# Optimization experiments

Hardware: AMD Instinct MI355X
Metric: run time of the kernel (lower is better)

## Reference

```python
import jax, jax.numpy as jnp
import numpy as np
import math

B, N, M = 128, 16, 32
D_OBS, D_OUT = 128, 128            # obs_input_dim, obs_output_dim (== obs_output_dim_other)
D_OA, D_AV = 136, 128              # obs_act_input_dim, obs_act_output_dim
D_OBS_O, D_OA_O, D_AV_O = 128, 136, 128
D_FINAL_IN, D_HID, D_FINAL_OUT = 256, 64, 1
N_ACT = 8


def setup_inputs() -> dict:
    key = jax.random.key(0)
    ks = jax.random.split(key, 16)
    s = 0.05
    return {
        "states": jax.random.normal(ks[0], (B, N, D_OBS), jnp.float32),
        "policies": jax.random.uniform(ks[1], (B, N, N_ACT), jnp.float32),
        "actions": jax.random.uniform(ks[2], (B, N, N_ACT), jnp.float32),
        "states_other": jax.random.normal(ks[3], (B, M, D_OBS_O), jnp.float32),
        "actions_other": jax.random.uniform(ks[4], (B, M, N_ACT), jnp.float32),
        # weights stored as [in, out] (torch Linear applies x @ W.T)
        "Wk": jax.random.normal(ks[5], (D_OBS, D_OUT), jnp.float32) * s,
        "Wq": jax.random.normal(ks[6], (D_OBS, D_OUT), jnp.float32) * s,
        "Wv": jax.random.normal(ks[7], (D_OA, D_AV), jnp.float32) * s,
        "Wk_o": jax.random.normal(ks[8], (D_OBS_O, D_OUT), jnp.float32) * s,
        "Wq_o": jax.random.normal(ks[9], (D_OBS, D_OUT), jnp.float32) * s,
        "Wv_o": jax.random.normal(ks[10], (D_OA_O, D_AV_O), jnp.float32) * s,
        "W1": jax.random.normal(ks[11], (D_FINAL_IN, D_HID), jnp.float32) * s,
        "W2": jax.random.normal(ks[12], (D_HID, D_FINAL_OUT), jnp.float32) * s,
    }


def reference(states, policies, actions, states_other, actions_other,
              Wk, Wq, Wv, Wk_o, Wq_o, Wv_o, W1, W2):
    d_k = float(D_OUT)
    d_k_o = float(D_OUT)  # d_k_obs_other = obs_output_dim_other

    obs_actions = jnp.concatenate([states, actions], axis=-1)   # [B,N,D_OA]
    obs_policy = jnp.concatenate([states, policies], axis=-1)   # [B,N,D_OA]

    k = states @ Wk                                             # [B,N,D_OUT]
    q = states @ Wq
    score = jnp.einsum('bid,bjd->bij', q, k)                    # [B,N,N]
    # torch softmaxes over the key axis (after reshape gymnastics)
    weight = jax.nn.softmax(score / math.sqrt(d_k), axis=-1)    # [B,N,N]
    ret_weight = weight

    # oap[b,j,k] = obs_policy[b,k] if j==k else obs_actions[b,k]
    eye = jnp.eye(N, dtype=states.dtype)[None, :, :, None]      # [1,N,N,1]
    oap = eye * obs_policy[:, None, :, :] + (1.0 - eye) * obs_actions[:, None, :, :]  # [B,N,N,D_OA]
    av = jnp.tanh(oap @ Wv)                                     # [B,N(j),N(k),D_AV]

    # torch: repeat av over a new agent axis i, multiply by weight[b,i,k], sum over k
    wav = jnp.einsum('bik,bjkd->bijd', weight, av)              # [B,N,N,D_AV]

    obs_actions_other = jnp.concatenate([states_other, actions_other], axis=-1)  # [B,M,D_OA_O]
    k_o = states_other @ Wk_o                                   # [B,M,D_OUT]
    q_o = states @ Wq_o                                         # [B,N,D_OUT]
    av_o = jnp.tanh(obs_actions_other @ Wv_o)                   # [B,M,D_AV_O]

    score_o = jnp.einsum('bid,bmd->bim', q_o, k_o)              # [B,N,M]
    # torch softmax dim=-2: over the agent axis (faithful, even if unusual)
    weight_o = jax.nn.softmax(score_o / math.sqrt(d_k_o), axis=1)  # [B,N,M]
    wav_o = jnp.einsum('bim,bmd->bid', weight_o, av_o)          # [B,N,D_AV_O]
    wav_o_b = jnp.broadcast_to(wav_o[:, :, None, :], (wav_o.shape[0], N, N, D_AV_O))

    node = jnp.concatenate([wav, wav_o_b], axis=-1)             # [B,N,N,256]
    h = jax.nn.leaky_relu(node @ W1)                            # [B,N,N,64]
    value = h @ W2                                              # [B,N,N,1]
    return value, ret_weight, weight_o[..., None]
```

## Files before the change

kernel.cpp:

```cpp
#include <hip/hip_runtime.h>
#include <math.h>

#define NB 128
#define NN 16
#define MM 32
#define DD 128
#define NACT 8
#define HH 64

#define WS_W  0
#define WS_V  32768
#define WS_US 163840
#define WS_UO 294912
#define WS_FLOATS (WS_UO + 131072)

__device__ float g_ws[WS_FLOATS];

#define A_ST 0
#define A_Q  2112
#define A_K  4224
#define A_AA 6336
#define A_DF 8448
#define A_P  10560
#define A_W  11648
#define A_AC 11920
#define A_PO 12048
#define B_ST  0
#define B_STO 2112
#define B_QO  6336
#define B_KOT 8448
#define B_AVO 12672
#define B_PO  16896
#define B_WO  19072
#define B_AO  19600
#define SM_FLOATS 19856

__device__ __forceinline__ float4 tanh4(float4 v) {
    float4 r; r.x = tanhf(v.x); r.y = tanhf(v.y); r.z = tanhf(v.z); r.w = tanhf(v.w); return r;
}
__device__ __forceinline__ void fma4(float4& a, float s, const float4& w) {
    a.x += s * w.x; a.y += s * w.y; a.z += s * w.z; a.w += s * w.w;
}

__launch_bounds__(512, 1)
__global__ void k_sides(const float* __restrict__ states,   const float* __restrict__ policies,
                        const float* __restrict__ actions,  const float* __restrict__ states_o,
                        const float* __restrict__ actions_o,
                        const float* __restrict__ Wq,  const float* __restrict__ Wk,
                        const float* __restrict__ Wv,  const float* __restrict__ Wqo,
                        const float* __restrict__ Wko, const float* __restrict__ Wvo,
                        const float* __restrict__ W1,
                        float* __restrict__ out) {
    __shared__ float sm[SM_FLOATS];
    const int b = blockIdx.x >> 1;
    const int side = blockIdx.x & 1;
    const int t = threadIdx.x;
    const float scale = 0.08838834764831845f;

    if (side == 0) {
        {
            int row = t >> 5, c4 = (t & 31) * 4;
            *(float4*)&sm[A_ST + row * 132 + c4] = *(const float4*)(states + b * 2048 + row * 128 + c4);
            if (t < 128) sm[A_AC + t] = actions [b * 128 + t];
            else if (t < 256) sm[A_PO + (t - 128)] = policies[b * 128 + (t - 128)];
        }
        __syncthreads();
        {
            const int i = t >> 5, c4 = (t & 31) * 4;
            float4 aq = {0,0,0,0}, ak = {0,0,0,0}, av = {0,0,0,0};
            #pragma unroll 4
            for (int kk = 0; kk < DD; ++kk) {
                float x = sm[A_ST + i * 132 + kk];
                fma4(aq, x, *(const float4*)(Wq + kk * 128 + c4));
                fma4(ak, x, *(const float4*)(Wk + kk * 128 + c4));
                fma4(av, x, *(const float4*)(Wv + kk * 128 + c4));
            }
            float4 aa = av, ap = av;
            #pragma unroll
            for (int kk = 0; kk < NACT; ++kk) {
                float4 wv = *(const float4*)(Wv + (DD + kk) * 128 + c4);
                fma4(aa, sm[A_AC + i * NACT + kk], wv);
                fma4(ap, sm[A_PO + i * NACT + kk], wv);
            }
            aa = tanh4(aa); ap = tanh4(ap);
            float4 df; df.x = ap.x - aa.x; df.y = ap.y - aa.y; df.z = ap.z - aa.z; df.w = ap.w - aa.w;
            *(float4*)&sm[A_Q  + i * 132 + c4] = aq;
            *(float4*)&sm[A_K  + i * 132 + c4] = ak;
            *(float4*)&sm[A_AA + i * 132 + c4] = aa;
            *(float4*)&sm[A_DF + i * 132 + c4] = df;
        }
        __syncthreads();
        if (t < 256) {
            int i = t >> 4, j = t & 15;
            float acc = 0.f;
            #pragma unroll 8
            for (int d = 0; d < DD; ++d) acc += sm[A_Q + i * 132 + d] * sm[A_K + j * 132 + d];
            sm[A_W + i * 17 + j] = acc * scale;
        } else {
            int tt = t - 256, i = tt >> 4, h4 = (tt & 15) * 4;
            float4 accp = {0,0,0,0}, accv = {0,0,0,0};
            #pragma unroll 4
            for (int kk = 0; kk < DD; ++kk) {
                float4 w4 = *(const float4*)(W1 + kk * HH + h4);
                fma4(accp, sm[A_AA + i * 132 + kk], w4);
                fma4(accv, sm[A_DF + i * 132 + kk], w4);
            }
            *(float4*)&sm[A_P + i * 68 + h4] = accp;
            *(float4*)(g_ws + WS_V + b * 1024 + i * 64 + h4) = accv;
        }
        __syncthreads();
        if (t < NN) {
            float mx = -1e30f;
            #pragma unroll
            for (int j = 0; j < NN; ++j) mx = fmaxf(mx, sm[A_W + t * 17 + j]);
            float e[NN], sum = 0.f;
            #pragma unroll
            for (int j = 0; j < NN; ++j) { e[j] = expf(sm[A_W + t * 17 + j] - mx); sum += e[j]; }
            float inv = 1.f / sum;
            #pragma unroll
            for (int j = 0; j < NN; ++j) sm[A_W + t * 17 + j] = e[j] * inv;
        }
        __syncthreads();
        if (t < 256) {
            float wv = sm[A_W + (t >> 4) * 17 + (t & 15)];
            out[NB * 256 + b * 256 + t] = wv;
            g_ws[WS_W + b * 256 + t] = wv;
        }
        {
            int i = t >> 5, h2 = (t & 31) * 2;
            float u0 = 0.f, u1 = 0.f;
            #pragma unroll
            for (int k = 0; k < NN; ++k) {
                float wv = sm[A_W + i * 17 + k];
                u0 += wv * sm[A_P + k * 68 + h2];
                u1 += wv * sm[A_P + k * 68 + h2 + 1];
            }
            *(float2*)(g_ws + WS_US + b * 1024 + i * 64 + h2) = make_float2(u0, u1);
        }
    } else {
        {
            int row = t >> 5, c4 = (t & 31) * 4;
            *(float4*)&sm[B_ST + row * 132 + c4] = *(const float4*)(states + b * 2048 + row * 128 + c4);
            int i2 = t + 512, row2 = (i2 >> 5) - 16, c42 = (i2 & 31) * 4;
            *(float4*)&sm[B_STO + row2 * 132 + c42] = *(const float4*)(states_o + b * 4096 + row2 * 128 + c42);
            int i3 = t + 1024, row3 = (i3 >> 5) - 32, c43 = (i3 & 31) * 4;
            *(float4*)&sm[B_STO + (row3 + 16) * 132 + c43] = *(const float4*)(states_o + b * 4096 + (row3 + 16) * 128 + c43);
            if (t < 256) sm[B_AO + t] = actions_o[b * 256 + t];
        }
        __syncthreads();
        {
            const int r = t >> 5, c4 = (t & 31) * 4;
            float4 aqo = {0,0,0,0}, ak0 = {0,0,0,0}, ak1 = {0,0,0,0}, av0 = {0,0,0,0}, av1 = {0,0,0,0};
            #pragma unroll 2
            for (int kk = 0; kk < DD; ++kk) {
                float xs = sm[B_ST  + r * 132 + kk];
                float x0 = sm[B_STO + r * 132 + kk];
                float x1 = sm[B_STO + (r + 16) * 132 + kk];
                float4 wq4 = *(const float4*)(Wqo + kk * 128 + c4);
                float4 wk4 = *(const float4*)(Wko + kk * 128 + c4);
                float4 wv4 = *(const float4*)(Wvo + kk * 128 + c4);
                fma4(aqo, xs, wq4);
                fma4(ak0, x0, wk4); fma4(ak1, x1, wk4);
                fma4(av0, x0, wv4); fma4(av1, x1, wv4);
            }
            #pragma unroll
            for (int kk = 0; kk < NACT; ++kk) {
                float4 wv4 = *(const float4*)(Wvo + (DD + kk) * 128 + c4);
                fma4(av0, sm[B_AO + r * NACT + kk], wv4);
                fma4(av1, sm[B_AO + (r + 16) * NACT + kk], wv4);
            }
            av0 = tanh4(av0); av1 = tanh4(av1);
            *(float4*)&sm[B_QO  + r * 132 + c4] = aqo;
            *(float4*)&sm[B_AVO + r * 132 + c4] = av0;
            *(float4*)&sm[B_AVO + (r + 16) * 132 + c4] = av1;
            sm[B_KOT + (c4 + 0) * 33 + r] = ak0.x; sm[B_KOT + (c4 + 1) * 33 + r] = ak0.y;
            sm[B_KOT + (c4 + 2) * 33 + r] = ak0.z; sm[B_KOT + (c4 + 3) * 33 + r] = ak0.w;
            sm[B_KOT + (c4 + 0) * 33 + r + 16] = ak1.x; sm[B_KOT + (c4 + 1) * 33 + r + 16] = ak1.y;
            sm[B_KOT + (c4 + 2) * 33 + r + 16] = ak1.z; sm[B_KOT + (c4 + 3) * 33 + r + 16] = ak1.w;
        }
        __syncthreads();
        {
            int i = t >> 5, m = t & 31;
            float acc = 0.f;
            #pragma unroll 8
            for (int d = 0; d < DD; ++d) acc += sm[B_QO + i * 132 + d] * sm[B_KOT + d * 33 + m];
            sm[B_WO + i * 33 + m] = acc * scale;
        }
        __syncthreads();
        if (t < MM) {
            float mx = -1e30f;
            #pragma unroll
            for (int i = 0; i < NN; ++i) mx = fmaxf(mx, sm[B_WO + i * 33 + t]);
            float e[NN], sum = 0.f;
            #pragma unroll
            for (int i = 0; i < NN; ++i) { e[i] = expf(sm[B_WO + i * 33 + t] - mx); sum += e[i]; }
            float inv = 1.f / sum;
            #pragma unroll
            for (int i = 0; i < NN; ++i) sm[B_WO + i * 33 + t] = e[i] * inv;
        }
        __syncthreads();
        {
            int r = t >> 4, h4 = (t & 15) * 4;
            float4 acc = {0,0,0,0};
            #pragma unroll 4
            for (int kk = 0; kk < DD; ++kk) {
                float4 w4 = *(const float4*)(W1 + (DD + kk) * HH + h4);
                fma4(acc, sm[B_AVO + r * 132 + kk], w4);
            }
            *(float4*)&sm[B_PO + r * 68 + h4] = acc;
        }
        __syncthreads();
        out[2 * NB * 256 + b * 512 + t] = sm[B_WO + (t >> 5) * 33 + (t & 31)];
        {
            int i = t >> 5, h2 = (t & 31) * 2;
            float u0 = 0.f, u1 = 0.f;
            #pragma unroll
            for (int m = 0; m < MM; ++m) {
                float wv = sm[B_WO + i * 33 + m];
                u0 += wv * sm[B_PO + m * 68 + h2];
                u1 += wv * sm[B_PO + m * 68 + h2 + 1];
            }
            *(float2*)(g_ws + WS_UO + b * 1024 + i * 64 + h2) = make_float2(u0, u1);
        }
    }
}

__launch_bounds__(256, 4)
__global__ void k_fin(const float* __restrict__ W2, float* __restrict__ out) {
    __shared__ float s_U[16 * 68];
    __shared__ float s_V[16 * 68];
    __shared__ float s_w[16 * 17];
    __shared__ float s_W2[HH];
    const int b = blockIdx.x, t = threadIdx.x;

    s_w[(t >> 4) * 17 + (t & 15)] = g_ws[WS_W + b * 256 + t];
    #pragma unroll
    for (int u = 0; u < 4; ++u) {
        int idx = t + u * 256;
        int i = idx >> 6, h = idx & 63;
        s_U[i * 68 + h] = g_ws[WS_US + b * 1024 + idx] + g_ws[WS_UO + b * 1024 + idx];
        s_V[i * 68 + h] = g_ws[WS_V + b * 1024 + idx];
    }
    if (t < HH) s_W2[t] = W2[t];
    __syncthreads();

    int i = t >> 4, j = t & 15;
    float wij = s_w[i * 17 + j];
    float acc = 0.f;
    #pragma unroll
    for (int h = 0; h < HH; ++h) {
        float x = s_U[i * 68 + h] + wij * s_V[j * 68 + h];
        x = (x > 0.f) ? x : 0.01f * x;
        acc += x * s_W2[h];
    }
    out[b * 256 + t] = acc;
}

extern "C" void kernel_launch(void* const* d_in, const int* in_sizes, int n_in,
                              void* d_out, int out_size, void* d_ws, size_t ws_size,
                              hipStream_t stream) {
    const float* states    = (const float*)d_in[0];
    const float* policies  = (const float*)d_in[1];
    const float* actions   = (const float*)d_in[2];
    const float* states_o  = (const float*)d_in[3];
    const float* actions_o = (const float*)d_in[4];
    const float* Wk        = (const float*)d_in[5];
    const float* Wq        = (const float*)d_in[6];
    const float* Wv        = (const float*)d_in[7];
    const float* Wk_o      = (const float*)d_in[8];
    const float* Wq_o      = (const float*)d_in[9];
    const float* Wv_o      = (const float*)d_in[10];
    const float* W1        = (const float*)d_in[11];
    const float* W2        = (const float*)d_in[12];
    float* out = (float*)d_out;

    hipLaunchKernelGGL(k_sides, dim3(256), dim3(512), 0, stream,
                       states, policies, actions, states_o, actions_o,
                       Wq, Wk, Wv, Wq_o, Wk_o, Wv_o, W1, out);
    hipLaunchKernelGGL(k_fin, dim3(128), dim3(256), 0, stream, W2, out);
}
```

Baseline: 118.2 us.

## Split per-batch work into four independent units and move weighted sums to finisher

The main kernel now launches 512 blocks of 256 threads, four units per batch (self attention, self values, other attention, other values), instead of 256 blocks of 512 threads with two sides. Each unit computes more rows per thread, so every weight load is reused across several rows. The softmax-weighted mixing of projected values (U = w·P + w_o·P_o) moves into the finisher kernel, which removes the dependency between attention and value work inside one block. The cost is more workspace traffic (P, P_o and w_o are written and reread) and a heavier finisher with an extra barrier.

Result: faster. 102.2 us (-13.6%).

```diff
diff --git a/kernel.cpp b/kernel.cpp
--- a/kernel.cpp
+++ b/kernel.cpp
@@ -9,31 +9,13 @@
 #define HH 64
 
 #define WS_W  0
-#define WS_V  32768
-#define WS_US 163840
-#define WS_UO 294912
-#define WS_FLOATS (WS_UO + 131072)
+#define WS_WO 32768
+#define WS_P  98304
+#define WS_V  229376
+#define WS_PO 360448
+#define WS_FLOATS 622592
 
 __device__ float g_ws[WS_FLOATS];
-
-#define A_ST 0
-#define A_Q  2112
-#define A_K  4224
-#define A_AA 6336
-#define A_DF 8448
-#define A_P  10560
-#define A_W  11648
-#define A_AC 11920
-#define A_PO 12048
-#define B_ST  0
-#define B_STO 2112
-#define B_QO  6336
-#define B_KOT 8448
-#define B_AVO 12672
-#define B_PO  16896
-#define B_WO  19072
-#define B_AO  19600
-#define SM_FLOATS 19856
 
 __device__ __forceinline__ float4 tanh4(float4 v) {
     float4 r; r.x = tanhf(v.x); r.y = tanhf(v.y); r.z = tanhf(v.z); r.w = tanhf(v.w); return r;
@@ -42,218 +24,300 @@
     a.x += s * w.x; a.y += s * w.y; a.z += s * w.z; a.w += s * w.w;
 }
 
-__launch_bounds__(512, 1)
-__global__ void k_sides(const float* __restrict__ states,   const float* __restrict__ policies,
-                        const float* __restrict__ actions,  const float* __restrict__ states_o,
-                        const float* __restrict__ actions_o,
-                        const float* __restrict__ Wq,  const float* __restrict__ Wk,
-                        const float* __restrict__ Wv,  const float* __restrict__ Wqo,
-                        const float* __restrict__ Wko, const float* __restrict__ Wvo,
-                        const float* __restrict__ W1,
-                        float* __restrict__ out) {
-    __shared__ float sm[SM_FLOATS];
-    const int b = blockIdx.x >> 1;
-    const int side = blockIdx.x & 1;
+__launch_bounds__(256, 2)
+__global__ void k_main(const float* __restrict__ states,   const float* __restrict__ policies,
+                       const float* __restrict__ actions,  const float* __restrict__ states_o,
+                       const float* __restrict__ actions_o,
+                       const float* __restrict__ Wq,  const float* __restrict__ Wk,
+                       const float* __restrict__ Wv,  const float* __restrict__ Wqo,
+                       const float* __restrict__ Wko, const float* __restrict__ Wvo,
+                       const float* __restrict__ W1,  float* __restrict__ out) {
+    __shared__ float sm[13200];
+    const int unit = blockIdx.x >> 7;
+    const int b = blockIdx.x & 127;
     const int t = threadIdx.x;
     const float scale = 0.08838834764831845f;
 
-    if (side == 0) {
+    if (unit == 0) {
+        float* s_st = sm;
+        float* s_q  = sm + 2112;
+        float* s_k  = sm + 4224;
+        float* s_w  = sm + 6336;
         {
             int row = t >> 5, c4 = (t & 31) * 4;
-            *(float4*)&sm[A_ST + row * 132 + c4] = *(const float4*)(states + b * 2048 + row * 128 + c4);
-            if (t < 128) sm[A_AC + t] = actions [b * 128 + t];
-            else if (t < 256) sm[A_PO + (t - 128)] = policies[b * 128 + (t - 128)];
-        }
-        __syncthreads();
-        {
-            const int i = t >> 5, c4 = (t & 31) * 4;
-            float4 aq = {0,0,0,0}, ak = {0,0,0,0}, av = {0,0,0,0};
+            *(float4*)&s_st[row * 132 + c4] = *(const float4*)(states + b * 2048 + row * 128 + c4);
+            int t2 = t + 256, row2 = t2 >> 5, c42 = (t2 & 31) * 4;
+            *(float4*)&s_st[row2 * 132 + c42] = *(const float4*)(states + b * 2048 + row2 * 128 + c42);
+        }
+        __syncthreads();
+        {
+            const int p = t >> 5, c4 = (t & 31) * 4;
+            float4 q0 = {0,0,0,0}, q1 = {0,0,0,0}, k0 = {0,0,0,0}, k1 = {0,0,0,0};
             #pragma unroll 4
             for (int kk = 0; kk < DD; ++kk) {
-                float x = sm[A_ST + i * 132 + kk];
-                fma4(aq, x, *(const float4*)(Wq + kk * 128 + c4));
-                fma4(ak, x, *(const float4*)(Wk + kk * 128 + c4));
-                fma4(av, x, *(const float4*)(Wv + kk * 128 + c4));
-            }
-            float4 aa = av, ap = av;
-            #pragma unroll
-            for (int kk = 0; kk < NACT; ++kk) {
-                float4 wv = *(const float4*)(Wv + (DD + kk) * 128 + c4);
-                fma4(aa, sm[A_AC + i * NACT + kk], wv);
-                fma4(ap, sm[A_PO + i * NACT + kk], wv);
-            }
-            aa = tanh4(aa); ap = tanh4(ap);
-            float4 df; df.x = ap.x - aa.x; df.y = ap.y - aa.y; df.z = ap.z - aa.z; df.w = ap.w - aa.w;
-            *(float4*)&sm[A_Q  + i * 132 + c4] = aq;
-            *(float4*)&sm[A_K  + i * 132 + c4] = ak;
-            *(float4*)&sm[A_AA + i * 132 + c4] = aa;
-            *(float4*)&sm[A_DF + i * 132 + c4] = df;
-        }
-        __syncthreads();
-        if (t < 256) {
+                float x0 = s_st[(2 * p) * 132 + kk], x1 = s_st[(2 * p + 1) * 132 + kk];
+                float4 wq = *(const float4*)(Wq + kk * 128 + c4);
+                float4 wk = *(const float4*)(Wk + kk * 128 + c4);
+                fma4(q0, x0, wq); fma4(q1, x1, wq);
+                fma4(k0, x0, wk); fma4(k1, x1, wk);
+            }
+            *(float4*)&s_q[(2 * p) * 132 + c4] = q0; *(float4*)&s_q[(2 * p + 1) * 132 + c4] = q1;
+            *(float4*)&s_k[(2 * p) * 132 + c4] = k0; *(float4*)&s_k[(2 * p + 1) * 132 + c4] = k1;
+        }
+        __syncthreads();
+        {
             int i = t >> 4, j = t & 15;
             float acc = 0.f;
             #pragma unroll 8
-            for (int d = 0; d < DD; ++d) acc += sm[A_Q + i * 132 + d] * sm[A_K + j * 132 + d];
-            sm[A_W + i * 17 + j] = acc * scale;
-        } else {
-            int tt = t - 256, i = tt >> 4, h4 = (tt & 15) * 4;
-            float4 accp = {0,0,0,0}, accv = {0,0,0,0};
-            #pragma unroll 4
-            for (int kk = 0; kk < DD; ++kk) {
-                float4 w4 = *(const float4*)(W1 + kk * HH + h4);
-                fma4(accp, sm[A_AA + i * 132 + kk], w4);
-                fma4(accv, sm[A_DF + i * 132 + kk], w4);
-            }
-            *(float4*)&sm[A_P + i * 68 + h4] = accp;
-            *(float4*)(g_ws + WS_V + b * 1024 + i * 64 + h4) = accv;
+            for (int d = 0; d < DD; ++d) acc += s_q[i * 132 + d] * s_k[j * 132 + d];
+            s_w[i * 17 + j] = acc * scale;
         }
         __syncthreads();
         if (t < NN) {
             float mx = -1e30f;
             #pragma unroll
-            for (int j = 0; j < NN; ++j) mx = fmaxf(mx, sm[A_W + t * 17 + j]);
+            for (int j = 0; j < NN; ++j) mx = fmaxf(mx, s_w[t * 17 + j]);
             float e[NN], sum = 0.f;
             #pragma unroll
-            for (int j = 0; j < NN; ++j) { e[j] = expf(sm[A_W + t * 17 + j] - mx); sum += e[j]; }
+            for (int j = 0; j < NN; ++j) { e[j] = expf(s_w[t * 17 + j] - mx); sum += e[j]; }
             float inv = 1.f / sum;
             #pragma unroll
-            for (int j = 0; j < NN; ++j) sm[A_W + t * 17 + j] = e[j] * inv;
-        }
-        __syncthreads();
-        if (t < 256) {
-            float wv = sm[A_W + (t >> 4) * 17 + (t & 15)];
+            for (int j = 0; j < NN; ++j) s_w[t * 17 + j] = e[j] * inv;
+        }
+        __syncthreads();
+        {
+            float wv = s_w[(t >> 4) * 17 + (t & 15)];
             out[NB * 256 + b * 256 + t] = wv;
             g_ws[WS_W + b * 256 + t] = wv;
         }
-        {
-            int i = t >> 5, h2 = (t & 31) * 2;
-            float u0 = 0.f, u1 = 0.f;
-            #pragma unroll
-            for (int k = 0; k < NN; ++k) {
-                float wv = sm[A_W + i * 17 + k];
-                u0 += wv * sm[A_P + k * 68 + h2];
-                u1 += wv * sm[A_P + k * 68 + h2 + 1];
-            }
-            *(float2*)(g_ws + WS_US + b * 1024 + i * 64 + h2) = make_float2(u0, u1);
-        }
-    } else {
+    } else if (unit == 1) {
+        float* s_st = sm;
+        float* s_aa = sm + 2112;
+        float* s_df = sm + 4224;
+        float* s_ac = sm + 6336;
+        float* s_po = sm + 6464;
         {
             int row = t >> 5, c4 = (t & 31) * 4;
-            *(float4*)&sm[B_ST + row * 132 + c4] = *(const float4*)(states + b * 2048 + row * 128 + c4);
-            int i2 = t + 512, row2 = (i2 >> 5) - 16, c42 = (i2 & 31) * 4;
-            *(float4*)&sm[B_STO + row2 * 132 + c42] = *(const float4*)(states_o + b * 4096 + row2 * 128 + c42);
-            int i3 = t + 1024, row3 = (i3 >> 5) - 32, c43 = (i3 & 31) * 4;
-            *(float4*)&sm[B_STO + (row3 + 16) * 132 + c43] = *(const float4*)(states_o + b * 4096 + (row3 + 16) * 128 + c43);
-            if (t < 256) sm[B_AO + t] = actions_o[b * 256 + t];
-        }
-        __syncthreads();
-        {
-            const int r = t >> 5, c4 = (t & 31) * 4;
-            float4 aqo = {0,0,0,0}, ak0 = {0,0,0,0}, ak1 = {0,0,0,0}, av0 = {0,0,0,0}, av1 = {0,0,0,0};
-            #pragma unroll 2
-            for (int kk = 0; kk < DD; ++kk) {
-                float xs = sm[B_ST  + r * 132 + kk];
-                float x0 = sm[B_STO + r * 132 + kk];
-                float x1 = sm[B_STO + (r + 16) * 132 + kk];
-                float4 wq4 = *(const float4*)(Wqo + kk * 128 + c4);
-                float4 wk4 = *(const float4*)(Wko + kk * 128 + c4);
-                float4 wv4 = *(const float4*)(Wvo + kk * 128 + c4);
-                fma4(aqo, xs, wq4);
-                fma4(ak0, x0, wk4); fma4(ak1, x1, wk4);
-                fma4(av0, x0, wv4); fma4(av1, x1, wv4);
-            }
-            #pragma unroll
-            for (int kk = 0; kk < NACT; ++kk) {
-                float4 wv4 = *(const float4*)(Wvo + (DD + kk) * 128 + c4);
-                fma4(av0, sm[B_AO + r * NACT + kk], wv4);
-                fma4(av1, sm[B_AO + (r + 16) * NACT + kk], wv4);
-            }
-            av0 = tanh4(av0); av1 = tanh4(av1);
-            *(float4*)&sm[B_QO  + r * 132 + c4] = aqo;
-            *(float4*)&sm[B_AVO + r * 132 + c4] = av0;
-            *(float4*)&sm[B_AVO + (r + 16) * 132 + c4] = av1;
-            sm[B_KOT + (c4 + 0) * 33 + r] = ak0.x; sm[B_KOT + (c4 + 1) * 33 + r] = ak0.y;
-            sm[B_KOT + (c4 + 2) * 33 + r] = ak0.z; sm[B_KOT + (c4 + 3) * 33 + r] = ak0.w;
-            sm[B_KOT + (c4 + 0) * 33 + r + 16] = ak1.x; sm[B_KOT + (c4 + 1) * 33 + r + 16] = ak1.y;
-            sm[B_KOT + (c4 + 2) * 33 + r + 16] = ak1.z; sm[B_KOT + (c4 + 3) * 33 + r + 16] = ak1.w;
+            *(float4*)&s_st[row * 132 + c4] = *(const float4*)(states + b * 2048 + row * 128 + c4);
+            int t2 = t + 256, row2 = t2 >> 5, c42 = (t2 & 31) * 4;
+            *(float4*)&s_st[row2 * 132 + c42] = *(const float4*)(states + b * 2048 + row2 * 128 + c42);
+            if (t < 128) {
+                s_ac[t] = actions [b * 128 + t];
+                s_po[t] = policies[b * 128 + t];
+            }
+        }
+        __syncthreads();
+        {
+            const int p = t >> 5, c4 = (t & 31) * 4;
+            float4 a0 = {0,0,0,0}, a1 = {0,0,0,0};
+            #pragma unroll 8
+            for (int kk = 0; kk < DD; ++kk) {
+                float4 wv = *(const float4*)(Wv + kk * 128 + c4);
+                fma4(a0, s_st[(2 * p) * 132 + kk], wv);
+                fma4(a1, s_st[(2 * p + 1) * 132 + kk], wv);
+            }
+            float4 aa0 = a0, aa1 = a1, ap0 = a0, ap1 = a1;
+            #pragma unroll
+            for (int k = 0; k < NACT; ++k) {
+                float4 wv = *(const float4*)(Wv + (DD + k) * 128 + c4);
+                fma4(aa0, s_ac[(2 * p) * 8 + k], wv); fma4(aa1, s_ac[(2 * p + 1) * 8 + k], wv);
+                fma4(ap0, s_po[(2 * p) * 8 + k], wv); fma4(ap1, s_po[(2 * p + 1) * 8 + k], wv);
+            }
+            aa0 = tanh4(aa0); aa1 = tanh4(aa1); ap0 = tanh4(ap0); ap1 = tanh4(ap1);
+            float4 d0, d1;
+            d0.x = ap0.x - aa0.x; d0.y = ap0.y - aa0.y; d0.z = ap0.z - aa0.z; d0.w = ap0.w - aa0.w;
+            d1.x = ap1.x - aa1.x; d1.y = ap1.y - aa1.y; d1.z = ap1.z - aa1.z; d1.w = ap1.w - aa1.w;
+            *(float4*)&s_aa[(2 * p) * 132 + c4] = aa0; *(float4*)&s_aa[(2 * p + 1) * 132 + c4] = aa1;
+            *(float4*)&s_df[(2 * p) * 132 + c4] = d0;  *(float4*)&s_df[(2 * p + 1) * 132 + c4] = d1;
+        }
+        __syncthreads();
+        {
+            const int i = t >> 4, h4 = (t & 15) * 4;
+            float4 pa = {0,0,0,0}, va = {0,0,0,0};
+            #pragma unroll 8
+            for (int kk = 0; kk < DD; ++kk) {
+                float4 w4 = *(const float4*)(W1 + kk * HH + h4);
+                fma4(pa, s_aa[i * 132 + kk], w4);
+                fma4(va, s_df[i * 132 + kk], w4);
+            }
+            *(float4*)(g_ws + WS_P + b * 1024 + i * 64 + h4) = pa;
+            *(float4*)(g_ws + WS_V + b * 1024 + i * 64 + h4) = va;
+        }
+    } else if (unit == 2) {
+        float* s_st  = sm;
+        float* s_qo  = sm + 2112;
+        float* s_sto = sm + 4224;
+        float* s_koT = sm + 8448;
+        float* s_wo  = sm + 12672;
+        {
+            int row = t >> 5, c4 = (t & 31) * 4;
+            *(float4*)&s_st[row * 132 + c4] = *(const float4*)(states + b * 2048 + row * 128 + c4);
+            int t2 = t + 256, row2 = t2 >> 5, c42 = (t2 & 31) * 4;
+            *(float4*)&s_st[row2 * 132 + c42] = *(const float4*)(states + b * 2048 + row2 * 128 + c42);
+            #pragma unroll
+            for (int u = 0; u < 4; ++u) {
+                int f = t + u * 256, r = f >> 5, cc = (f & 31) * 4;
+                *(float4*)&s_sto[r * 132 + cc] = *(const float4*)(states_o + b * 4096 + r * 128 + cc);
+            }
+        }
+        __syncthreads();
+        {
+            const int p = t >> 5, c4 = (t & 31) * 4;
+            float4 g0 = {0,0,0,0}, g1 = {0,0,0,0};
+            float4 o0 = {0,0,0,0}, o1 = {0,0,0,0}, o2 = {0,0,0,0}, o3 = {0,0,0,0};
+            #pragma unroll 4
+            for (int kk = 0; kk < DD; ++kk) {
+                float4 wq = *(const float4*)(Wqo + kk * 128 + c4);
+                float4 wk = *(const float4*)(Wko + kk * 128 + c4);
+                fma4(g0, s_st[(2 * p) * 132 + kk], wq);
+                fma4(g1, s_st[(2 * p + 1) * 132 + kk], wq);
+                fma4(o0, s_sto[(4 * p) * 132 + kk], wk);
+                fma4(o1, s_sto[(4 * p + 1) * 132 + kk], wk);
+                fma4(o2, s_sto[(4 * p + 2) * 132 + kk], wk);
+                fma4(o3, s_sto[(4 * p + 3) * 132 + kk], wk);
+            }
+            *(float4*)&s_qo[(2 * p) * 132 + c4] = g0;
+            *(float4*)&s_qo[(2 * p + 1) * 132 + c4] = g1;
+            s_koT[(c4+0)*33 + 4*p]   = o0.x; s_koT[(c4+1)*33 + 4*p]   = o0.y; s_koT[(c4+2)*33 + 4*p]   = o0.z; s_koT[(c4+3)*33 + 4*p]   = o0.w;
+            s_koT[(c4+0)*33 + 4*p+1] = o1.x; s_koT[(c4+1)*33 + 4*p+1] = o1.y; s_koT[(c4+2)*33 + 4*p+1] = o1.z; s_koT[(c4+3)*33 + 4*p+1] = o1.w;
+            s_koT[(c4+0)*33 + 4*p+2] = o2.x; s_koT[(c4+1)*33 + 4*p+2] = o2.y; s_koT[(c4+2)*33 + 4*p+2] = o2.z; s_koT[(c4+3)*33 + 4*p+2] = o2.w;
+            s_koT[(c4+0)*33 + 4*p+3] = o3.x; s_koT[(c4+1)*33 + 4*p+3] = o3.y; s_koT[(c4+2)*33 + 4*p+3] = o3.z; s_koT[(c4+3)*33 + 4*p+3] = o3.w;
         }
         __syncthreads();
         {
             int i = t >> 5, m = t & 31;
-            float acc = 0.f;
-            #pragma unroll 8
-            for (int d = 0; d < DD; ++d) acc += sm[B_QO + i * 132 + d] * sm[B_KOT + d * 33 + m];
-            sm[B_WO + i * 33 + m] = acc * scale;
+            float a0 = 0.f, a1 = 0.f;
+            #pragma unroll 8
+            for (int d = 0; d < DD; ++d) {
+                float kv = s_koT[d * 33 + m];
+                a0 += s_qo[i * 132 + d] * kv;
+                a1 += s_qo[(i + 8) * 132 + d] * kv;
+            }
+            s_wo[i * 33 + m] = a0 * scale;
+            s_wo[(i + 8) * 33 + m] = a1 * scale;
         }
         __syncthreads();
         if (t < MM) {
             float mx = -1e30f;
             #pragma unroll
-            for (int i = 0; i < NN; ++i) mx = fmaxf(mx, sm[B_WO + i * 33 + t]);
+            for (int i = 0; i < NN; ++i) mx = fmaxf(mx, s_wo[i * 33 + t]);
             float e[NN], sum = 0.f;
             #pragma unroll
-            for (int i = 0; i < NN; ++i) { e[i] = expf(sm[B_WO + i * 33 + t] - mx); sum += e[i]; }
+            for (int i = 0; i < NN; ++i) { e[i] = expf(s_wo[i * 33 + t] - mx); sum += e[i]; }
             float inv = 1.f / sum;
             #pragma unroll
-            for (int i = 0; i < NN; ++i) sm[B_WO + i * 33 + t] = e[i] * inv;
-        }
-        __syncthreads();
-        {
-            int r = t >> 4, h4 = (t & 15) * 4;
-            float4 acc = {0,0,0,0};
-            #pragma unroll 4
+            for (int i = 0; i < NN; ++i) s_wo[i * 33 + t] = e[i] * inv;
+        }
+        __syncthreads();
+        {
+            float w0 = s_wo[(t >> 5) * 33 + (t & 31)];
+            float w1 = s_wo[((t + 256) >> 5) * 33 + (t & 31)];
+            out[2 * NB * 256 + b * 512 + t] = w0;
+            out[2 * NB * 256 + b * 512 + 256 + t] = w1;
+            g_ws[WS_WO + b * 512 + t] = w0;
+            g_ws[WS_WO + b * 512 + 256 + t] = w1;
+        }
+    } else {
+        float* s_sto = sm;
+        float* s_avo = sm + 4224;
+        float* s_ao  = sm + 8448;
+        {
+            #pragma unroll
+            for (int u = 0; u < 4; ++u) {
+                int f = t + u * 256, r = f >> 5, cc = (f & 31) * 4;
+                *(float4*)&s_sto[r * 132 + cc] = *(const float4*)(states_o + b * 4096 + r * 128 + cc);
+            }
+            s_ao[t] = actions_o[b * 256 + t];
+        }
+        __syncthreads();
+        {
+            const int p = t >> 5, c4 = (t & 31) * 4;
+            float4 v0 = {0,0,0,0}, v1 = {0,0,0,0}, v2 = {0,0,0,0}, v3 = {0,0,0,0};
+            #pragma unroll 8
+            for (int kk = 0; kk < DD; ++kk) {
+                float4 wv = *(const float4*)(Wvo + kk * 128 + c4);
+                fma4(v0, s_sto[(4 * p) * 132 + kk], wv);
+                fma4(v1, s_sto[(4 * p + 1) * 132 + kk], wv);
+                fma4(v2, s_sto[(4 * p + 2) * 132 + kk], wv);
+                fma4(v3, s_sto[(4 * p + 3) * 132 + kk], wv);
+            }
+            #pragma unroll
+            for (int k = 0; k < NACT; ++k) {
+                float4 wv = *(const float4*)(Wvo + (DD + k) * 128 + c4);
+                fma4(v0, s_ao[(4 * p) * 8 + k], wv);
+                fma4(v1, s_ao[(4 * p + 1) * 8 + k], wv);
+                fma4(v2, s_ao[(4 * p + 2) * 8 + k], wv);
+                fma4(v3, s_ao[(4 * p + 3) * 8 + k], wv);
+            }
+            *(float4*)&s_avo[(4 * p) * 132 + c4]     = tanh4(v0);
+            *(float4*)&s_avo[(4 * p + 1) * 132 + c4] = tanh4(v1);
+            *(float4*)&s_avo[(4 * p + 2) * 132 + c4] = tanh4(v2);
+            *(float4*)&s_avo[(4 * p + 3) * 132 + c4] = tanh4(v3);
+        }
+        __syncthreads();
+        {
+            const int r = t >> 4, h4 = (t & 15) * 4;
+            float4 p0 = {0,0,0,0}, p1 = {0,0,0,0};
+            #pragma unroll 8
             for (int kk = 0; kk < DD; ++kk) {
                 float4 w4 = *(const float4*)(W1 + (DD + kk) * HH + h4);
-                fma4(acc, sm[B_AVO + r * 132 + kk], w4);
-            }
-            *(float4*)&sm[B_PO + r * 68 + h4] = acc;
-        }
-        __syncthreads();
-        out[2 * NB * 256 + b * 512 + t] = sm[B_WO + (t >> 5) * 33 + (t & 31)];
-        {
-            int i = t >> 5, h2 = (t & 31) * 2;
-            float u0 = 0.f, u1 = 0.f;
-            #pragma unroll
-            for (int m = 0; m < MM; ++m) {
-                float wv = sm[B_WO + i * 33 + m];
-                u0 += wv * sm[B_PO + m * 68 + h2];
-                u1 += wv * sm[B_PO + m * 68 + h2 + 1];
-            }
-            *(float2*)(g_ws + WS_UO + b * 1024 + i * 64 + h2) = make_float2(u0, u1);
+                fma4(p0, s_avo[r * 132 + kk], w4);
+                fma4(p1, s_avo[(r + 16) * 132 + kk], w4);
+            }
+            *(float4*)(g_ws + WS_PO + b * 2048 + r * 64 + h4) = p0;
+            *(float4*)(g_ws + WS_PO + b * 2048 + (r + 16) * 64 + h4) = p1;
         }
     }
 }
 
-__launch_bounds__(256, 4)
+__launch_bounds__(256, 2)
 __global__ void k_fin(const float* __restrict__ W2, float* __restrict__ out) {
-    __shared__ float s_U[16 * 68];
-    __shared__ float s_V[16 * 68];
-    __shared__ float s_w[16 * 17];
+    __shared__ float s_w [16 * 17];
+    __shared__ float s_wo[16 * 33];
+    __shared__ float s_P [16 * 64];
+    __shared__ float s_Po[32 * 64];
+    __shared__ float s_V [16 * 68];
+    __shared__ float s_U [16 * 68];
     __shared__ float s_W2[HH];
     const int b = blockIdx.x, t = threadIdx.x;
 
     s_w[(t >> 4) * 17 + (t & 15)] = g_ws[WS_W + b * 256 + t];
+    s_wo[(t >> 5) * 33 + (t & 31)] = g_ws[WS_WO + b * 512 + t];
+    s_wo[((t + 256) >> 5) * 33 + (t & 31)] = g_ws[WS_WO + b * 512 + 256 + t];
+    ((float4*)s_P)[t] = ((const float4*)(g_ws + WS_P + b * 1024))[t];
+    ((float4*)s_Po)[t] = ((const float4*)(g_ws + WS_PO + b * 2048))[t];
+    ((float4*)s_Po)[t + 256] = ((const float4*)(g_ws + WS_PO + b * 2048))[t + 256];
     #pragma unroll
     for (int u = 0; u < 4; ++u) {
         int idx = t + u * 256;
-        int i = idx >> 6, h = idx & 63;
-        s_U[i * 68 + h] = g_ws[WS_US + b * 1024 + idx] + g_ws[WS_UO + b * 1024 + idx];
-        s_V[i * 68 + h] = g_ws[WS_V + b * 1024 + idx];
+        s_V[(idx >> 6) * 68 + (idx & 63)] = g_ws[WS_V + b * 1024 + idx];
     }
     if (t < HH) s_W2[t] = W2[t];
     __syncthreads();
 
-    int i = t >> 4, j = t & 15;
-    float wij = s_w[i * 17 + j];
-    float acc = 0.f;
-    #pragma unroll
-    for (int h = 0; h < HH; ++h) {
-        float x = s_U[i * 68 + h] + wij * s_V[j * 68 + h];
-        x = (x > 0.f) ? x : 0.01f * x;
-        acc += x * s_W2[h];
+    {
+        int i = t >> 4, h4 = (t & 15) * 4;
+        float4 u = {0,0,0,0};
+        #pragma unroll
+        for (int k = 0; k < NN; ++k) fma4(u, s_w[i * 17 + k], *(const float4*)&s_P[k * 64 + h4]);
+        #pragma unroll
+        for (int m = 0; m < MM; ++m) fma4(u, s_wo[i * 33 + m], *(const float4*)&s_Po[m * 64 + h4]);
+        *(float4*)&s_U[i * 68 + h4] = u;
     }
-    out[b * 256 + t] = acc;
+    __syncthreads();
+
+    {
+        int i = t >> 4, j = t & 15;
+        float wij = s_w[i * 17 + j];
+        float acc = 0.f;
+        #pragma unroll
+        for (int h = 0; h < HH; ++h) {
+            float x = s_U[i * 68 + h] + wij * s_V[j * 68 + h];
+            x = (x > 0.f) ? x : 0.01f * x;
+            acc += x * s_W2[h];
+        }
+        out[b * 256 + t] = acc;
+    }
 }
 
 extern "C" void kernel_launch(void* const* d_in, const int* in_sizes, int n_in,
@@ -274,7 +338,7 @@
     const float* W2        = (const float*)d_in[12];
     float* out = (float*)d_out;
 
-    hipLaunchKernelGGL(k_sides, dim3(256), dim3(512), 0, stream,
+    hipLaunchKernelGGL(k_main, dim3(512), dim3(256), 0, stream,
                        states, policies, actions, states_o, actions_o,
                        Wq, Wk, Wv, Wq_o, Wk_o, Wv_o, W1, out);
     hipLaunchKernelGGL(k_fin, dim3(128), dim3(256), 0, stream, W2, out);
```

## Split per-batch work into four independent block units and move mixing into finisher

Applied to the files above, without the earlier changes.

The main kernel now launches four block types per batch (Q/K attention, value projection, other-agent attention, other-agent value projection) instead of two, so twice as many blocks share the work and each carries fewer dependent stages. The weight-times-projection mixing (U) moves into the finisher kernel, which now reads raw projections and both weight matrices from workspace. Softmaxes use wave shuffles instead of a serial per-thread loop. In exchange, the input tiles are loaded more than once, more data passes through the global workspace, and the finisher does more work.

Result: faster. 114.6 us (-3.1%).

```diff
diff --git a/kernel.cpp b/kernel.cpp
--- a/kernel.cpp
+++ b/kernel.cpp
@@ -9,85 +9,65 @@
 #define HH 64
 
 #define WS_W  0
-#define WS_V  32768
-#define WS_US 163840
-#define WS_UO 294912
-#define WS_FLOATS (WS_UO + 131072)
+#define WS_WO 32768
+#define WS_P  98304
+#define WS_V  229376
+#define WS_PO 360448
+#define WS_FLOATS 622592
 
 __device__ float g_ws[WS_FLOATS];
+
+__device__ __forceinline__ float4 tanh4(float4 v) {
+    float4 r; r.x = tanhf(v.x); r.y = tanhf(v.y); r.z = tanhf(v.z); r.w = tanhf(v.w); return r;
+}
+__device__ __forceinline__ void fma4(float4& a, float s, const float4& w) {
+    a.x += s * w.x; a.y += s * w.y; a.z += s * w.z; a.w += s * w.w;
+}
 
 #define A_ST 0
 #define A_Q  2112
 #define A_K  4224
-#define A_AA 6336
-#define A_DF 8448
-#define A_P  10560
-#define A_W  11648
-#define A_AC 11920
-#define A_PO 12048
+#define A2_AA 2112
+#define A2_DF 4224
+#define A2_AC 6336
+#define A2_PO 6464
 #define B_ST  0
-#define B_STO 2112
-#define B_QO  6336
+#define B_QO  2112
+#define B_STO 4224
 #define B_KOT 8448
-#define B_AVO 12672
-#define B_PO  16896
-#define B_WO  19072
-#define B_AO  19600
-#define SM_FLOATS 19856
-
-__device__ __forceinline__ float4 tanh4(float4 v) {
-    float4 r; r.x = tanhf(v.x); r.y = tanhf(v.y); r.z = tanhf(v.z); r.w = tanhf(v.w); return r;
-}
-__device__ __forceinline__ void fma4(float4& a, float s, const float4& w) {
-    a.x += s * w.x; a.y += s * w.y; a.z += s * w.z; a.w += s * w.w;
-}
-
-__launch_bounds__(512, 1)
-__global__ void k_sides(const float* __restrict__ states,   const float* __restrict__ policies,
-                        const float* __restrict__ actions,  const float* __restrict__ states_o,
-                        const float* __restrict__ actions_o,
-                        const float* __restrict__ Wq,  const float* __restrict__ Wk,
-                        const float* __restrict__ Wv,  const float* __restrict__ Wqo,
-                        const float* __restrict__ Wko, const float* __restrict__ Wvo,
-                        const float* __restrict__ W1,
-                        float* __restrict__ out) {
-    __shared__ float sm[SM_FLOATS];
-    const int b = blockIdx.x >> 1;
-    const int side = blockIdx.x & 1;
+#define B_WO  12672
+#define B2_STO 0
+#define B2_AVO 4224
+#define B2_AO  8448
+
+__launch_bounds__(512, 2)
+__global__ void k_main(const float* __restrict__ states,   const float* __restrict__ policies,
+                       const float* __restrict__ actions,  const float* __restrict__ states_o,
+                       const float* __restrict__ actions_o,
+                       const float* __restrict__ Wq,  const float* __restrict__ Wk,
+                       const float* __restrict__ Wv,  const float* __restrict__ Wqo,
+                       const float* __restrict__ Wko, const float* __restrict__ Wvo,
+                       const float* __restrict__ W1,  float* __restrict__ out) {
+    __shared__ float sm[13200];
+    const int unit = blockIdx.x >> 7;
+    const int b = blockIdx.x & 127;
     const int t = threadIdx.x;
+    const int row = t >> 5, c4 = (t & 31) * 4;
     const float scale = 0.08838834764831845f;
 
-    if (side == 0) {
-        {
-            int row = t >> 5, c4 = (t & 31) * 4;
-            *(float4*)&sm[A_ST + row * 132 + c4] = *(const float4*)(states + b * 2048 + row * 128 + c4);
-            if (t < 128) sm[A_AC + t] = actions [b * 128 + t];
-            else if (t < 256) sm[A_PO + (t - 128)] = policies[b * 128 + (t - 128)];
-        }
-        __syncthreads();
-        {
-            const int i = t >> 5, c4 = (t & 31) * 4;
-            float4 aq = {0,0,0,0}, ak = {0,0,0,0}, av = {0,0,0,0};
-            #pragma unroll 4
+    if (unit == 0) {
+        *(float4*)&sm[A_ST + row * 132 + c4] = *(const float4*)(states + b * 2048 + row * 128 + c4);
+        __syncthreads();
+        {
+            float4 q = {0,0,0,0}, k = {0,0,0,0};
+            #pragma unroll 8
             for (int kk = 0; kk < DD; ++kk) {
-                float x = sm[A_ST + i * 132 + kk];
-                fma4(aq, x, *(const float4*)(Wq + kk * 128 + c4));
-                fma4(ak, x, *(const float4*)(Wk + kk * 128 + c4));
-                fma4(av, x, *(const float4*)(Wv + kk * 128 + c4));
-            }
-            float4 aa = av, ap = av;
-            #pragma unroll
-            for (int kk = 0; kk < NACT; ++kk) {
-                float4 wv = *(const float4*)(Wv + (DD + kk) * 128 + c4);
-                fma4(aa, sm[A_AC + i * NACT + kk], wv);
-                fma4(ap, sm[A_PO + i * NACT + kk], wv);
-            }
-            aa = tanh4(aa); ap = tanh4(ap);
-            float4 df; df.x = ap.x - aa.x; df.y = ap.y - aa.y; df.z = ap.z - aa.z; df.w = ap.w - aa.w;
-            *(float4*)&sm[A_Q  + i * 132 + c4] = aq;
-            *(float4*)&sm[A_K  + i * 132 + c4] = ak;
-            *(float4*)&sm[A_AA + i * 132 + c4] = aa;
-            *(float4*)&sm[A_DF + i * 132 + c4] = df;
+                float x = sm[A_ST + row * 132 + kk];
+                fma4(q, x, *(const float4*)(Wq + kk * 128 + c4));
+                fma4(k, x, *(const float4*)(Wk + kk * 128 + c4));
+            }
+            *(float4*)&sm[A_Q + row * 132 + c4] = q;
+            *(float4*)&sm[A_K + row * 132 + c4] = k;
         }
         __syncthreads();
         if (t < 256) {
@@ -95,88 +75,75 @@
             float acc = 0.f;
             #pragma unroll 8
             for (int d = 0; d < DD; ++d) acc += sm[A_Q + i * 132 + d] * sm[A_K + j * 132 + d];
-            sm[A_W + i * 17 + j] = acc * scale;
-        } else {
-            int tt = t - 256, i = tt >> 4, h4 = (tt & 15) * 4;
-            float4 accp = {0,0,0,0}, accv = {0,0,0,0};
+            acc *= scale;
+            float mx = acc;
+            #pragma unroll
+            for (int msk = 8; msk >= 1; msk >>= 1) mx = fmaxf(mx, __shfl_xor(mx, msk, 16));
+            float e = expf(acc - mx);
+            float sum = e;
+            #pragma unroll
+            for (int msk = 8; msk >= 1; msk >>= 1) sum += __shfl_xor(sum, msk, 16);
+            float wv = e / sum;
+            out[NB * 256 + b * 256 + t] = wv;
+            g_ws[WS_W + b * 256 + t] = wv;
+        }
+    } else if (unit == 1) {
+        *(float4*)&sm[A_ST + row * 132 + c4] = *(const float4*)(states + b * 2048 + row * 128 + c4);
+        if (t < 128) sm[A2_AC + t] = actions [b * 128 + t];
+        else if (t < 256) sm[A2_PO + (t - 128)] = policies[b * 128 + (t - 128)];
+        __syncthreads();
+        {
+            float4 a = {0,0,0,0};
+            #pragma unroll 8
+            for (int kk = 0; kk < DD; ++kk)
+                fma4(a, sm[A_ST + row * 132 + kk], *(const float4*)(Wv + kk * 128 + c4));
+            float4 aa = a, ap = a;
+            #pragma unroll
+            for (int k = 0; k < NACT; ++k) {
+                float4 wv = *(const float4*)(Wv + (DD + k) * 128 + c4);
+                fma4(aa, sm[A2_AC + row * 8 + k], wv);
+                fma4(ap, sm[A2_PO + row * 8 + k], wv);
+            }
+            aa = tanh4(aa); ap = tanh4(ap);
+            float4 df; df.x = ap.x - aa.x; df.y = ap.y - aa.y; df.z = ap.z - aa.z; df.w = ap.w - aa.w;
+            *(float4*)&sm[A2_AA + row * 132 + c4] = aa;
+            *(float4*)&sm[A2_DF + row * 132 + c4] = df;
+        }
+        __syncthreads();
+        {
+            int tt = t & 255, i = tt >> 4, h4 = (tt & 15) * 4;
+            const float* src = (t < 256) ? sm + A2_AA : sm + A2_DF;
+            float* dst = (t < 256) ? g_ws + WS_P + b * 1024 : g_ws + WS_V + b * 1024;
+            float4 acc = {0,0,0,0};
+            #pragma unroll 8
+            for (int kk = 0; kk < DD; ++kk)
+                fma4(acc, src[i * 132 + kk], *(const float4*)(W1 + kk * HH + h4));
+            *(float4*)(dst + i * 64 + h4) = acc;
+        }
+    } else if (unit == 2) {
+        *(float4*)&sm[B_ST + row * 132 + c4] = *(const float4*)(states + b * 2048 + row * 128 + c4);
+        #pragma unroll
+        for (int u = 0; u < 2; ++u) {
+            int f = t + u * 512, r = f >> 5, cc = (f & 31) * 4;
+            *(float4*)&sm[B_STO + r * 132 + cc] = *(const float4*)(states_o + b * 4096 + r * 128 + cc);
+        }
+        __syncthreads();
+        {
+            float4 g = {0,0,0,0}, o0 = {0,0,0,0}, o1 = {0,0,0,0};
             #pragma unroll 4
             for (int kk = 0; kk < DD; ++kk) {
-                float4 w4 = *(const float4*)(W1 + kk * HH + h4);
-                fma4(accp, sm[A_AA + i * 132 + kk], w4);
-                fma4(accv, sm[A_DF + i * 132 + kk], w4);
-            }
-            *(float4*)&sm[A_P + i * 68 + h4] = accp;
-            *(float4*)(g_ws + WS_V + b * 1024 + i * 64 + h4) = accv;
-        }
-        __syncthreads();
-        if (t < NN) {
-            float mx = -1e30f;
-            #pragma unroll
-            for (int j = 0; j < NN; ++j) mx = fmaxf(mx, sm[A_W + t * 17 + j]);
-            float e[NN], sum = 0.f;
-            #pragma unroll
-            for (int j = 0; j < NN; ++j) { e[j] = expf(sm[A_W + t * 17 + j] - mx); sum += e[j]; }
-            float inv = 1.f / sum;
-            #pragma unroll
-            for (int j = 0; j < NN; ++j) sm[A_W + t * 17 + j] = e[j] * inv;
-        }
-        __syncthreads();
-        if (t < 256) {
-            float wv = sm[A_W + (t >> 4) * 17 + (t & 15)];
-            out[NB * 256 + b * 256 + t] = wv;
-            g_ws[WS_W + b * 256 + t] = wv;
-        }
-        {
-            int i = t >> 5, h2 = (t & 31) * 2;
-            float u0 = 0.f, u1 = 0.f;
-            #pragma unroll
-            for (int k = 0; k < NN; ++k) {
-                float wv = sm[A_W + i * 17 + k];
-                u0 += wv * sm[A_P + k * 68 + h2];
-                u1 += wv * sm[A_P + k * 68 + h2 + 1];
-            }
-            *(float2*)(g_ws + WS_US + b * 1024 + i * 64 + h2) = make_float2(u0, u1);
-        }
-    } else {
-        {
-            int row = t >> 5, c4 = (t & 31) * 4;
-            *(float4*)&sm[B_ST + row * 132 + c4] = *(const float4*)(states + b * 2048 + row * 128 + c4);
-            int i2 = t + 512, row2 = (i2 >> 5) - 16, c42 = (i2 & 31) * 4;
-            *(float4*)&sm[B_STO + row2 * 132 + c42] = *(const float4*)(states_o + b * 4096 + row2 * 128 + c42);
-            int i3 = t + 1024, row3 = (i3 >> 5) - 32, c43 = (i3 & 31) * 4;
-            *(float4*)&sm[B_STO + (row3 + 16) * 132 + c43] = *(const float4*)(states_o + b * 4096 + (row3 + 16) * 128 + c43);
-            if (t < 256) sm[B_AO + t] = actions_o[b * 256 + t];
-        }
-        __syncthreads();
-        {
-            const int r = t >> 5, c4 = (t & 31) * 4;
-            float4 aqo = {0,0,0,0}, ak0 = {0,0,0,0}, ak1 = {0,0,0,0}, av0 = {0,0,0,0}, av1 = {0,0,0,0};
-            #pragma unroll 2
-            for (int kk = 0; kk < DD; ++kk) {
-                float xs = sm[B_ST  + r * 132 + kk];
-                float x0 = sm[B_STO + r * 132 + kk];
-                float x1 = sm[B_STO + (r + 16) * 132 + kk];
-                float4 wq4 = *(const float4*)(Wqo + kk * 128 + c4);
-                float4 wk4 = *(const float4*)(Wko + kk * 128 + c4);
-                float4 wv4 = *(const float4*)(Wvo + kk * 128 + c4);
-                fma4(aqo, xs, wq4);
-                fma4(ak0, x0, wk4); fma4(ak1, x1, wk4);
-                fma4(av0, x0, wv4); fma4(av1, x1, wv4);
-            }
-            #pragma unroll
-            for (int kk = 0; kk < NACT; ++kk) {
-                float4 wv4 = *(const float4*)(Wvo + (DD + kk) * 128 + c4);
-                fma4(av0, sm[B_AO + r * NACT + kk], wv4);
-                fma4(av1, sm[B_AO + (r + 16) * NACT + kk], wv4);
-            }
-            av0 = tanh4(av0); av1 = tanh4(av1);
-            *(float4*)&sm[B_QO  + r * 132 + c4] = aqo;
-            *(float4*)&sm[B_AVO + r * 132 + c4] = av0;
-            *(float4*)&sm[B_AVO + (r + 16) * 132 + c4] = av1;
-            sm[B_KOT + (c4 + 0) * 33 + r] = ak0.x; sm[B_KOT + (c4 + 1) * 33 + r] = ak0.y;
-            sm[B_KOT + (c4 + 2) * 33 + r] = ak0.z; sm[B_KOT + (c4 + 3) * 33 + r] = ak0.w;
-            sm[B_KOT + (c4 + 0) * 33 + r + 16] = ak1.x; sm[B_KOT + (c4 + 1) * 33 + r + 16] = ak1.y;
-            sm[B_KOT + (c4 + 2) * 33 + r + 16] = ak1.z; sm[B_KOT + (c4 + 3) * 33 + r + 16] = ak1.w;
+                float xs = sm[B_ST  + row * 132 + kk];
+                float x0 = sm[B_STO + row * 132 + kk];
+                float x1 = sm[B_STO + (row + 16) * 132 + kk];
+                float4 wq = *(const float4*)(Wqo + kk * 128 + c4);
+                float4 wk = *(const float4*)(Wko + kk * 128 + c4);
+                fma4(g, xs, wq); fma4(o0, x0, wk); fma4(o1, x1, wk);
+            }
+            *(float4*)&sm[B_QO + row * 132 + c4] = g;
+            sm[B_KOT + (c4+0)*33 + row] = o0.x; sm[B_KOT + (c4+1)*33 + row] = o0.y;
+            sm[B_KOT + (c4+2)*33 + row] = o0.z; sm[B_KOT + (c4+3)*33 + row] = o0.w;
+            sm[B_KOT + (c4+0)*33 + row+16] = o1.x; sm[B_KOT + (c4+1)*33 + row+16] = o1.y;
+            sm[B_KOT + (c4+2)*33 + row+16] = o1.z; sm[B_KOT + (c4+3)*33 + row+16] = o1.w;
         }
         __syncthreads();
         {
@@ -187,73 +154,109 @@
             sm[B_WO + i * 33 + m] = acc * scale;
         }
         __syncthreads();
-        if (t < MM) {
-            float mx = -1e30f;
-            #pragma unroll
-            for (int i = 0; i < NN; ++i) mx = fmaxf(mx, sm[B_WO + i * 33 + t]);
-            float e[NN], sum = 0.f;
-            #pragma unroll
-            for (int i = 0; i < NN; ++i) { e[i] = expf(sm[B_WO + i * 33 + t] - mx); sum += e[i]; }
-            float inv = 1.f / sum;
-            #pragma unroll
-            for (int i = 0; i < NN; ++i) sm[B_WO + i * 33 + t] = e[i] * inv;
+        {
+            int m = t >> 4, i = t & 15;
+            float x = sm[B_WO + i * 33 + m];
+            float mx = x;
+            #pragma unroll
+            for (int msk = 8; msk >= 1; msk >>= 1) mx = fmaxf(mx, __shfl_xor(mx, msk, 16));
+            float e = expf(x - mx);
+            float sum = e;
+            #pragma unroll
+            for (int msk = 8; msk >= 1; msk >>= 1) sum += __shfl_xor(sum, msk, 16);
+            sm[B_WO + i * 33 + m] = e / sum;
+        }
+        __syncthreads();
+        {
+            float wv = sm[B_WO + (t >> 5) * 33 + (t & 31)];
+            out[2 * NB * 256 + b * 512 + t] = wv;
+            g_ws[WS_WO + b * 512 + t] = wv;
+        }
+    } else {
+        #pragma unroll
+        for (int u = 0; u < 2; ++u) {
+            int f = t + u * 512, r = f >> 5, cc = (f & 31) * 4;
+            *(float4*)&sm[B2_STO + r * 132 + cc] = *(const float4*)(states_o + b * 4096 + r * 128 + cc);
+        }
+        if (t < 256) sm[B2_AO + t] = actions_o[b * 256 + t];
+        __syncthreads();
+        {
+            float4 v0 = {0,0,0,0}, v1 = {0,0,0,0};
+            #pragma unroll 8
+            for (int kk = 0; kk < DD; ++kk) {
+                float4 wv = *(const float4*)(Wvo + kk * 128 + c4);
+                fma4(v0, sm[B2_STO + row * 132 + kk], wv);
+                fma4(v1, sm[B2_STO + (row + 16) * 132 + kk], wv);
+            }
+            #pragma unroll
+            for (int k = 0; k < NACT; ++k) {
+                float4 wv = *(const float4*)(Wvo + (DD + k) * 128 + c4);
+                fma4(v0, sm[B2_AO + row * 8 + k], wv);
+                fma4(v1, sm[B2_AO + (row + 16) * 8 + k], wv);
+            }
+            *(float4*)&sm[B2_AVO + row * 132 + c4]        = tanh4(v0);
+            *(float4*)&sm[B2_AVO + (row + 16) * 132 + c4] = tanh4(v1);
         }
         __syncthreads();
         {
             int r = t >> 4, h4 = (t & 15) * 4;
             float4 acc = {0,0,0,0};
-            #pragma unroll 4
-            for (int kk = 0; kk < DD; ++kk) {
-                float4 w4 = *(const float4*)(W1 + (DD + kk) * HH + h4);
-                fma4(acc, sm[B_AVO + r * 132 + kk], w4);
-            }
-            *(float4*)&sm[B_PO + r * 68 + h4] = acc;
-        }
-        __syncthreads();
-        out[2 * NB * 256 + b * 512 + t] = sm[B_WO + (t >> 5) * 33 + (t & 31)];
-        {
-            int i = t >> 5, h2 = (t & 31) * 2;
-            float u0 = 0.f, u1 = 0.f;
-            #pragma unroll
-            for (int m = 0; m < MM; ++m) {
-                float wv = sm[B_WO + i * 33 + m];
-                u0 += wv * sm[B_PO + m * 68 + h2];
-                u1 += wv * sm[B_PO + m * 68 + h2 + 1];
-            }
-            *(float2*)(g_ws + WS_UO + b * 1024 + i * 64 + h2) = make_float2(u0, u1);
-        }
-    }
-}
-
-__launch_bounds__(256, 4)
+            #pragma unroll 8
+            for (int kk = 0; kk < DD; ++kk)
+                fma4(acc, sm[B2_AVO + r * 132 + kk], *(const float4*)(W1 + (DD + kk) * HH + h4));
+            *(float4*)(g_ws + WS_PO + b * 2048 + r * 64 + h4) = acc;
+        }
+    }
+}
+
+__launch_bounds__(256, 2)
 __global__ void k_fin(const float* __restrict__ W2, float* __restrict__ out) {
-    __shared__ float s_U[16 * 68];
-    __shared__ float s_V[16 * 68];
-    __shared__ float s_w[16 * 17];
+    __shared__ float s_w [16 * 17];
+    __shared__ float s_wo[16 * 33];
+    __shared__ float s_P [16 * 64];
+    __shared__ float s_Po[32 * 64];
+    __shared__ float s_V [16 * 68];
+    __shared__ float s_U [16 * 68];
     __shared__ float s_W2[HH];
     const int b = blockIdx.x, t = threadIdx.x;
 
     s_w[(t >> 4) * 17 + (t & 15)] = g_ws[WS_W + b * 256 + t];
+    s_wo[(t >> 5) * 33 + (t & 31)] = g_ws[WS_WO + b * 512 + t];
+    s_wo[((t + 256) >> 5) * 33 + (t & 31)] = g_ws[WS_WO + b * 512 + 256 + t];
+    ((float4*)s_P)[t] = ((const float4*)(g_ws + WS_P + b * 1024))[t];
+    ((float4*)s_Po)[t] = ((const float4*)(g_ws + WS_PO + b * 2048))[t];
+    ((float4*)s_Po)[t + 256] = ((const float4*)(g_ws + WS_PO + b * 2048))[t + 256];
     #pragma unroll
     for (int u = 0; u < 4; ++u) {
         int idx = t + u * 256;
-        int i = idx >> 6, h = idx & 63;
-        s_U[i * 68 + h] = g_ws[WS_US + b * 1024 + idx] + g_ws[WS_UO + b * 1024 + idx];
-        s_V[i * 68 + h] = g_ws[WS_V + b * 1024 + idx];
+        s_V[(idx >> 6) * 68 + (idx & 63)] = g_ws[WS_V + b * 1024 + idx];
     }
     if (t < HH) s_W2[t] = W2[t];
     __syncthreads();
 
-    int i = t >> 4, j = t & 15;
-    float wij = s_w[i * 17 + j];
-    float acc = 0.f;
-    #pragma unroll
-    for (int h = 0; h < HH; ++h) {
-        float x = s_U[i * 68 + h] + wij * s_V[j * 68 + h];
-        x = (x > 0.f) ? x : 0.01f * x;
-        acc += x * s_W2[h];
-    }
-    out[b * 256 + t] = acc;
+    {
+        int i = t >> 4, h4 = (t & 15) * 4;
+        float4 u = {0,0,0,0};
+        #pragma unroll
+        for (int k = 0; k < NN; ++k) fma4(u, s_w[i * 17 + k], *(const float4*)&s_P[k * 64 + h4]);
+        #pragma unroll
+        for (int m = 0; m < MM; ++m) fma4(u, s_wo[i * 33 + m], *(const float4*)&s_Po[m * 64 + h4]);
+        *(float4*)&s_U[i * 68 + h4] = u;
+    }
+    __syncthreads();
+
+    {
+        int i = t >> 4, j = t & 15;
+        float wij = s_w[i * 17 + j];
+        float acc = 0.f;
+        #pragma unroll
+        for (int h = 0; h < HH; ++h) {
+            float x = s_U[i * 68 + h] + wij * s_V[j * 68 + h];
+            x = (x > 0.f) ? x : 0.01f * x;
+            acc += x * s_W2[h];
+        }
+        out[b * 256 + t] = acc;
+    }
 }
 
 extern "C" void kernel_launch(void* const* d_in, const int* in_sizes, int n_in,
@@ -274,7 +277,7 @@
     const float* W2        = (const float*)d_in[12];
     float* out = (float*)d_out;
 
-    hipLaunchKernelGGL(k_sides, dim3(256), dim3(512), 0, stream,
+    hipLaunchKernelGGL(k_main, dim3(512), dim3(512), 0, stream,
                        states, policies, actions, states_o, actions_o,
                        Wq, Wk, Wv, Wq_o, Wk_o, Wv_o, W1, out);
     hipLaunchKernelGGL(k_fin, dim3(128), dim3(256), 0, stream, W2, out);
```
